# Kernel tuning notes

Hardware: AMD Instinct MI355X
Metric: run time of the kernel (lower is better)

Reference implementation:

```python
import jax, jax.numpy as jnp
import numpy as np

N = 100000          # nodes
E = 600000          # edges (avg degree ~6, mesh graph)
C_IN = 6            # input features (xyz + normals)
H = 64              # hidden channels per PointTransformerConv
OUT = 10            # out_channels
NEG_SLOPE = 0.01    # F.leaky_relu default slope
IN_DIMS = [C_IN, C_IN + H, C_IN + 2 * H, C_IN + 3 * H]


def _lin(key, fin, fout):
    return jax.random.normal(key, (fin, fout), jnp.float32) / np.float32(np.sqrt(fin))


def setup_inputs() -> dict:
    key = jax.random.key(0)
    ks = jax.random.split(key, 40)
    inp = {
        "x": jax.random.normal(ks[0], (N, C_IN), jnp.float32),
        "edge_index": jax.random.randint(ks[1], (2, E), 0, N, jnp.int32),
    }
    k = 2
    for l, fin in enumerate(IN_DIMS, start=1):
        inp[f"w{l}_lin"] = _lin(ks[k], fin, H); k += 1   # value projection (bias=False)
        inp[f"w{l}_src"] = _lin(ks[k], fin, H); k += 1   # attention src projection
        inp[f"w{l}_dst"] = _lin(ks[k], fin, H); k += 1   # attention dst projection
        inp[f"w{l}_pos"] = _lin(ks[k], fin, H); k += 1   # positional MLP (Linear)
        inp[f"b{l}_pos"] = jnp.zeros((H,), jnp.float32)
    inp["w_mlp1"] = _lin(ks[k], C_IN + 4 * H, H); k += 1
    inp["b_mlp1"] = jnp.zeros((H,), jnp.float32)
    inp["w_mlp2"] = _lin(ks[k], H, OUT); k += 1
    inp["b_mlp2"] = jnp.zeros((OUT,), jnp.float32)
    return inp


def _ptconv(x, src, dst, w_lin, w_src, w_dst, w_pos, b_pos):
    """PointTransformerConv with x serving as both features and positions.
    message = softmax_i(a_dst[i] - a_src[j] + delta_ij) * (h[j] + delta_ij),
    delta_ij = pos_nn(x_i - x_j); sum-aggregated over incoming edges."""
    h = x @ w_lin                                   # [N,H] values
    a_src = x @ w_src                               # [N,H]
    a_dst = x @ w_dst                               # [N,H]
    delta = (x[dst] - x[src]) @ w_pos + b_pos       # [E,H] pos_nn(pos_i - pos_j)
    alpha = a_dst[dst] - a_src[src] + delta         # [E,H] per-edge, per-channel logits
    # numerically stable segment softmax over edges grouped by destination node
    amax = jax.ops.segment_max(alpha, dst, num_segments=N)      # [N,H]
    e = jnp.exp(alpha - amax[dst])                              # [E,H]
    denom = jax.ops.segment_sum(e, dst, num_segments=N)         # [N,H]
    w = e / (denom[dst] + 1e-16)                                # [E,H]
    return jax.ops.segment_sum(w * (h[src] + delta), dst, num_segments=N)  # [N,H]


def _forward(x, edge_index, ps):
    src, dst = edge_index[0], edge_index[1]
    lrelu = lambda v: jnp.where(v > 0, v, NEG_SLOPE * v)
    x1 = _ptconv(x, src, dst, *ps[0])
    x2 = lrelu(_ptconv(jnp.concatenate([x, x1], 1), src, dst, *ps[1]))
    x3 = lrelu(_ptconv(jnp.concatenate([x, x1, x2], 1), src, dst, *ps[2]))
    x4 = lrelu(_ptconv(jnp.concatenate([x, x1, x2, x3], 1), src, dst, *ps[3]))
    out = jnp.concatenate([x, x1, x2, x3, x4], 1)   # [N, 262]
    w_mlp1, b_mlp1, w_mlp2, b_mlp2 = ps[4]
    out = out @ w_mlp1 + b_mlp1                     # dropout = identity (eval mode)
    return out @ w_mlp2 + b_mlp2                    # [N, OUT]


def reference(x, edge_index,
              w1_lin, w1_src, w1_dst, w1_pos, b1_pos,
              w2_lin, w2_src, w2_dst, w2_pos, b2_pos,
              w3_lin, w3_src, w3_dst, w3_pos, b3_pos,
              w4_lin, w4_src, w4_dst, w4_pos, b4_pos,
              w_mlp1, b_mlp1, w_mlp2, b_mlp2):
    ps = [(w1_lin, w1_src, w1_dst, w1_pos, b1_pos),
          (w2_lin, w2_src, w2_dst, w2_pos, b2_pos),
          (w3_lin, w3_src, w3_dst, w3_pos, b3_pos),
          (w4_lin, w4_src, w4_dst, w4_pos, b4_pos),
          (w_mlp1, b_mlp1, w_mlp2, b_mlp2)]
    return _forward(x, edge_index, ps)
```

## Files before the change

### kernel.cpp

```cpp
#include <hip/hip_runtime.h>
#include <hip/hip_fp16.h>

#define NN 100000
#define EE 600000
#define XSB 288
#define SCAN_B 2048

typedef __attribute__((ext_vector_type(8))) short s16x8;
typedef __attribute__((ext_vector_type(4))) float f32x4;

__device__ inline unsigned short f2b(float f) {
    unsigned u = __float_as_uint(f);
    u += 0x7fffu + ((u >> 16) & 1u);
    return (unsigned short)(u >> 16);
}


__global__ void k_init_x(const float* __restrict__ x, unsigned short* __restrict__ xb) {
    int idx = blockIdx.x * 256 + threadIdx.x;
    if (idx < NN * 6) {
        int i = idx / 6, c = idx - i * 6;
        xb[(size_t)i * XSB + c] = f2b(x[idx]);
    }
}

__global__ void k_wconv(const float* __restrict__ wlin, const float* __restrict__ wsrc,
                        const float* __restrict__ wpos,
                        unsigned short* __restrict__ wt, int fin, int KP) {
    int idx = blockIdx.x * 256 + threadIdx.x;
    if (idx >= 192 * KP) return;
    int ks = idx / 6144;
    int rem = idx - ks * 6144;
    int col = rem >> 5, kk = rem & 31;
    int k = ks * 32 + kk;
    float val = 0.f;
    if (k < fin) {
        int m = col >> 6, c = col & 63;
        const float* W = (m == 0) ? wlin : (m == 1) ? wsrc : wpos;
        val = W[k * 64 + c];
    }
    wt[idx] = f2b(val);
}

__global__ void k_wconv1(const float* __restrict__ w1, unsigned short* __restrict__ wt) {
    int idx = blockIdx.x * 256 + threadIdx.x;
    if (idx >= 64 * 288) return;
    int col = idx / 288, k = idx - col * 288;
    wt[idx] = f2b((k < 262) ? w1[k * 64 + col] : 0.f);
}


__global__ void k_hist(const int* __restrict__ ei, int* __restrict__ deg) {
    int e = blockIdx.x * 256 + threadIdx.x;
    if (e < EE) atomicAdd(&deg[ei[EE + e]], 1);
}

__global__ void k_scan1(const int* __restrict__ deg, int* __restrict__ rowptr,
                        int* __restrict__ bsum) {
    __shared__ int sh[256];
    int b = blockIdx.x, t = threadIdx.x;
    int base = b * SCAN_B + t * 8;
    int vals[8];
    int s = 0;
#pragma unroll
    for (int j = 0; j < 8; j++) {
        int i = base + j;
        int d = (i < NN) ? deg[i] : 0;
        s += d;
        vals[j] = s;
    }
    sh[t] = s;
    __syncthreads();
    for (int off = 1; off < 256; off <<= 1) {
        int vv = (t >= off) ? sh[t - off] : 0;
        __syncthreads();
        sh[t] += vv;
        __syncthreads();
    }
    int excl = (t > 0) ? sh[t - 1] : 0;
#pragma unroll
    for (int j = 0; j < 8; j++) {
        int i = base + j;
        if (i < NN) rowptr[i + 1] = vals[j] + excl;
    }
    if (t == 255) bsum[b] = sh[255];
}

__global__ void k_scan2(int* __restrict__ bsum, int nb) {
    __shared__ int sh[256];
    int t = threadIdx.x;
    sh[t] = (t < nb) ? bsum[t] : 0;
    __syncthreads();
    for (int off = 1; off < 256; off <<= 1) {
        int vv = (t >= off) ? sh[t - off] : 0;
        __syncthreads();
        sh[t] += vv;
        __syncthreads();
    }
    if (t < nb) bsum[t] = sh[t];
}

__global__ void k_scan3(const int* __restrict__ deg, int* __restrict__ rowptr,
                        const int* __restrict__ bsum, int* __restrict__ cursor) {
    int b = blockIdx.x, t = threadIdx.x;
    int off = (b > 0) ? bsum[b - 1] : 0;
    int base = b * SCAN_B + t * 8;
#pragma unroll
    for (int j = 0; j < 8; j++) {
        int i = base + j;
        if (i < NN) {
            int incl = rowptr[i + 1] + off;
            rowptr[i + 1] = incl;
            cursor[i] = incl - deg[i];
        }
    }
    if (b == 0 && t == 0) rowptr[0] = 0;
}

__global__ void k_scatter(const int* __restrict__ ei, int* __restrict__ cursor,
                          int* __restrict__ csrc) {
    int e = blockIdx.x * 256 + threadIdx.x;
    if (e < EE) {
        int d = ei[EE + e];
        int pos = atomicAdd(&cursor[d], 1);
        csrc[pos] = ei[e];
    }
}


template <int KP>
__global__ __launch_bounds__(256) void k_projm(
    const unsigned short* __restrict__ xb, const unsigned short* __restrict__ wt,
    const float* __restrict__ bpos,
    __half2* __restrict__ vg, float* __restrict__ q) {
    __shared__ short wl[192 * 32];
    const int t = threadIdx.x;
    const int w = t >> 6, l = t & 63;
    const int lo = l & 15, hi = l >> 4;
    const int row_w = blockIdx.x * 64 + w * 16;

    f32x4 acc[12];
#pragma unroll
    for (int i = 0; i < 12; i++) acc[i] = (f32x4)0.f;

    const unsigned short* arow = xb + (size_t)(row_w + lo) * XSB;
#pragma unroll
    for (int ks = 0; ks < KP / 32; ks++) {
        __syncthreads();
        {
            const uint4* src = (const uint4*)wt + (size_t)ks * 768;
            uint4* dst = (uint4*)wl;
#pragma unroll
            for (int i = 0; i < 3; i++) dst[i * 256 + t] = src[i * 256 + t];
        }
        __syncthreads();
        s16x8 af = *(const s16x8*)(arow + ks * 32 + hi * 8);
#pragma unroll
        for (int ct = 0; ct < 12; ct++) {
            s16x8 bf = *(const s16x8*)&wl[(ct * 16 + lo) * 32 + hi * 8];
            acc[ct] = __builtin_amdgcn_mfma_f32_16x16x32_bf16(af, bf, acc[ct], 0, 0, 0);
        }
    }

#pragma unroll
    for (int r = 0; r < 4; r++) {
        int node = row_w + hi * 4 + r;
        if (node < NN) {
#pragma unroll
            for (int j = 0; j < 4; j++) {
                int c = j * 16 + lo;
                float h  = acc[0 + j][r];
                float as = acc[4 + j][r];
                float p  = acc[8 + j][r];
                size_t o = (size_t)node * 64 + c;
                vg[o] = __floats2half2_rn(as + p, h - p);
                q[o] = p + bpos[c];
            }
        }
    }
}


__global__ __launch_bounds__(256) void k_mlp1(
    const unsigned short* __restrict__ xb, const unsigned short* __restrict__ w1t,
    const float* __restrict__ b1, float* __restrict__ hid) {
    const int w = threadIdx.x >> 6, l = threadIdx.x & 63;
    const int lo = l & 15, hi = l >> 4;
    const int row_w = blockIdx.x * 256 + w * 64;

    f32x4 acc[4][4];
#pragma unroll
    for (int a = 0; a < 4; a++)
#pragma unroll
        for (int b = 0; b < 4; b++) acc[a][b] = (f32x4)0.f;

#pragma unroll
    for (int ks = 0; ks < 9; ks++) {
        const int k0 = ks * 32 + hi * 8;
        s16x8 bf[4];
#pragma unroll
        for (int ct = 0; ct < 4; ct++)
            bf[ct] = *(const s16x8*)(w1t + (size_t)(ct * 16 + lo) * 288 + k0);
#pragma unroll
        for (int rt = 0; rt < 4; rt++) {
            s16x8 af = *(const s16x8*)(xb + (size_t)(row_w + rt * 16 + lo) * XSB + k0);
#pragma unroll
            for (int ct = 0; ct < 4; ct++)
                acc[rt][ct] = __builtin_amdgcn_mfma_f32_16x16x32_bf16(af, bf[ct], acc[rt][ct], 0, 0, 0);
        }
    }

#pragma unroll
    for (int rt = 0; rt < 4; rt++) {
#pragma unroll
        for (int r = 0; r < 4; r++) {
            int node = row_w + rt * 16 + hi * 4 + r;
            if (node < NN) {
#pragma unroll
                for (int ct = 0; ct < 4; ct++) {
                    int c = ct * 16 + lo;
                    hid[(size_t)node * 64 + c] = acc[rt][ct][r] + b1[c];
                }
            }
        }
    }
}


template <int RELU>
__global__ __launch_bounds__(256) void k_edge(
    const __half2* __restrict__ vg, const float* __restrict__ q,
    const int* __restrict__ rowptr, const int* __restrict__ csrc,
    unsigned short* __restrict__ xb, int col) {
    int node = blockIdx.x * 4 + (threadIdx.x >> 6);
    int lane = threadIdx.x & 63;
    if (node >= NN) return;
    float ql = q[(size_t)node * 64 + lane];
    int b = rowptr[node], e = rowptr[node + 1];
    float d = 0.f, s1 = 0.f;
    for (int p0 = b; p0 < e; p0 += 8) {
        int cnt = e - p0;
        int sidx[8];
#pragma unroll
        for (int j = 0; j < 8; j++) {
            int pp = p0 + j;
            if (pp >= e) pp = e - 1;
            sidx[j] = csrc[pp];
        }
        __half2 hv[8];
#pragma unroll
        for (int j = 0; j < 8; j++)
            hv[j] = vg[(size_t)sidx[j] * 64 + lane];
#pragma unroll
        for (int j = 0; j < 8; j++) {
            float2 f = __half22float2(hv[j]);
            float ee = __expf(-f.x);
            if (j >= cnt) ee = 0.f;
            d += ee;
            s1 = fmaf(ee, f.y, s1);
        }
    }
    float o = (s1 + ql * d) / (d + 1e-16f);
    if (RELU) o = (o > 0.f) ? o : 0.01f * o;
    xb[(size_t)node * XSB + col + lane] = f2b(o);
}


__global__ __launch_bounds__(256) void k_mlp2(
    const float* __restrict__ hid, const float* __restrict__ w2,
    const float* __restrict__ b2, float* __restrict__ out) {
    int n = blockIdx.x * 256 + threadIdx.x;
    if (n >= NN) return;
    float acc[10];
#pragma unroll
    for (int o = 0; o < 10; o++) acc[o] = b2[o];
    for (int h = 0; h < 64; h++) {
        float hv = hid[(size_t)n * 64 + h];
#pragma unroll
        for (int o = 0; o < 10; o++) acc[o] += hv * w2[h * 10 + o];
    }
#pragma unroll
    for (int o = 0; o < 10; o++) out[(size_t)n * 10 + o] = acc[o];
}


extern "C" void kernel_launch(void* const* d_in, const int* in_sizes, int n_in,
                              void* d_out, int out_size, void* d_ws, size_t ws_size,
                              hipStream_t stream) {
    const float* x = (const float*)d_in[0];
    const int* ei = (const int*)d_in[1];
    const float* W[4][4];
    const float* BP[4];
    int base = 2;
    for (int l = 0; l < 4; l++) {
        for (int m = 0; m < 4; m++) W[l][m] = (const float*)d_in[base + m];
        BP[l] = (const float*)d_in[base + 4];
        base += 5;
    }
    const float* w1 = (const float*)d_in[22];
    const float* b1 = (const float*)d_in[23];
    const float* w2 = (const float*)d_in[24];
    const float* b2 = (const float*)d_in[25];

    char* wsp = (char*)d_ws;
    size_t off = 0;
    auto alloc = [&](size_t bytes) {
        void* p = wsp + off;
        off += (bytes + 255) & ~(size_t)255;
        return p;
    };
    unsigned short* xb = (unsigned short*)alloc((size_t)(NN + 256) * XSB * 2);
    __half2* vg = (__half2*)alloc((size_t)NN * 64 * 4);
    float* q = (float*)alloc((size_t)NN * 64 * 4);
    int* deg = (int*)alloc((size_t)NN * 4);
    int* rowptr = (int*)alloc((size_t)(NN + 1) * 4);
    int* cursor = (int*)alloc((size_t)NN * 4);
    int* bsum = (int*)alloc(1024 * 4);
    int* csrc = (int*)alloc((size_t)EE * 4);
    const int KPv[4] = {32, 96, 160, 224};
    const int FINv[4] = {6, 70, 134, 198};
    unsigned short* wt[4];
    for (int l = 0; l < 4; l++) wt[l] = (unsigned short*)alloc((size_t)192 * KPv[l] * 2);
    unsigned short* w1t = (unsigned short*)alloc((size_t)64 * 288 * 2);
    float* hid = q;

    hipMemsetAsync(deg, 0, (size_t)NN * 4, stream);
    k_init_x<<<(NN * 6 + 255) / 256, 256, 0, stream>>>(x, xb);
    for (int l = 0; l < 4; l++)
        k_wconv<<<(192 * KPv[l] + 255) / 256, 256, 0, stream>>>(
            W[l][0], W[l][1], W[l][3], wt[l], FINv[l], KPv[l]);
    k_wconv1<<<(64 * 288 + 255) / 256, 256, 0, stream>>>(w1, w1t);

    k_hist<<<(EE + 255) / 256, 256, 0, stream>>>(ei, deg);
    int nb = (NN + SCAN_B - 1) / SCAN_B;
    k_scan1<<<nb, 256, 0, stream>>>(deg, rowptr, bsum);
    k_scan2<<<1, 256, 0, stream>>>(bsum, nb);
    k_scan3<<<nb, 256, 0, stream>>>(deg, rowptr, bsum, cursor);
    k_scatter<<<(EE + 255) / 256, 256, 0, stream>>>(ei, cursor, csrc);

    const int gProj = (NN + 63) / 64;
    const int gEdge = (NN + 3) / 4;

    k_projm<32><<<gProj, 256, 0, stream>>>(xb, wt[0], BP[0], vg, q);
    k_edge<0><<<gEdge, 256, 0, stream>>>(vg, q, rowptr, csrc, xb, 6);
    k_projm<96><<<gProj, 256, 0, stream>>>(xb, wt[1], BP[1], vg, q);
    k_edge<1><<<gEdge, 256, 0, stream>>>(vg, q, rowptr, csrc, xb, 70);
    k_projm<160><<<gProj, 256, 0, stream>>>(xb, wt[2], BP[2], vg, q);
    k_edge<1><<<gEdge, 256, 0, stream>>>(vg, q, rowptr, csrc, xb, 134);
    k_projm<224><<<gProj, 256, 0, stream>>>(xb, wt[3], BP[3], vg, q);
    k_edge<1><<<gEdge, 256, 0, stream>>>(vg, q, rowptr, csrc, xb, 198);

    k_mlp1<<<(NN + 255) / 256, 256, 0, stream>>>(xb, w1t, b1, hid);
    k_mlp2<<<(NN + 255) / 256, 256, 0, stream>>>(hid, w2, b2, (float*)d_out);
}
```

Baseline: 330.0 us.

## Fuse setup kernels, fuse MLP layers, halve q precision, widen edge loads

Merges x conversion, all weight conversions and the degree memset into one setup launch. Fuses the second MLP into the first MFMA kernel using shuffle reductions, which removes the hidden-activation round trip through memory. Stores q in fp16, processes 32 rows per wave in the projection kernel so each shared-memory weight load is reused twice, and has the edge kernel gather 8-byte vectors with half-waves covering alternate edges. The fp16 q adds some rounding error.

```diff
diff --git a/kernel.cpp b/kernel.cpp
--- a/kernel.cpp
+++ b/kernel.cpp
@@ -15,20 +15,9 @@
     return (unsigned short)(u >> 16);
 }
 
-
-__global__ void k_init_x(const float* __restrict__ x, unsigned short* __restrict__ xb) {
-    int idx = blockIdx.x * 256 + threadIdx.x;
-    if (idx < NN * 6) {
-        int i = idx / 6, c = idx - i * 6;
-        xb[(size_t)i * XSB + c] = f2b(x[idx]);
-    }
-}
-
-__global__ void k_wconv(const float* __restrict__ wlin, const float* __restrict__ wsrc,
-                        const float* __restrict__ wpos,
-                        unsigned short* __restrict__ wt, int fin, int KP) {
-    int idx = blockIdx.x * 256 + threadIdx.x;
-    if (idx >= 192 * KP) return;
+__device__ inline void wconv_elem(int idx, int fin,
+                                  const float* wlin, const float* wsrc,
+                                  const float* wpos, unsigned short* wt) {
     int ks = idx / 6144;
     int rem = idx - ks * 6144;
     int col = rem >> 5, kk = rem & 31;
@@ -42,11 +31,44 @@
     wt[idx] = f2b(val);
 }
 
-__global__ void k_wconv1(const float* __restrict__ w1, unsigned short* __restrict__ wt) {
-    int idx = blockIdx.x * 256 + threadIdx.x;
-    if (idx >= 64 * 288) return;
-    int col = idx / 288, k = idx - col * 288;
-    wt[idx] = f2b((k < 262) ? w1[k * 64 + col] : 0.f);
+#define O0 600000
+#define O1 606144
+#define O2 624576
+#define O3 655296
+#define O4 698304
+#define O5 716736
+#define O6 816736
+
+__global__ __launch_bounds__(256) void k_setup(
+    const float* __restrict__ x,
+    const float* __restrict__ wl0, const float* __restrict__ ws0, const float* __restrict__ wp0,
+    const float* __restrict__ wl1, const float* __restrict__ ws1, const float* __restrict__ wp1,
+    const float* __restrict__ wl2, const float* __restrict__ ws2, const float* __restrict__ wp2,
+    const float* __restrict__ wl3, const float* __restrict__ ws3, const float* __restrict__ wp3,
+    const float* __restrict__ w1,
+    unsigned short* __restrict__ xb,
+    unsigned short* __restrict__ wt0, unsigned short* __restrict__ wt1,
+    unsigned short* __restrict__ wt2, unsigned short* __restrict__ wt3,
+    unsigned short* __restrict__ w1t, int* __restrict__ deg) {
+    int i = blockIdx.x * 256 + threadIdx.x;
+    if (i < O0) {
+        int n = i / 6, c = i - n * 6;
+        xb[(size_t)n * XSB + c] = f2b(x[i]);
+    } else if (i < O1) {
+        wconv_elem(i - O0, 6, wl0, ws0, wp0, wt0);
+    } else if (i < O2) {
+        wconv_elem(i - O1, 70, wl1, ws1, wp1, wt1);
+    } else if (i < O3) {
+        wconv_elem(i - O2, 134, wl2, ws2, wp2, wt2);
+    } else if (i < O4) {
+        wconv_elem(i - O3, 198, wl3, ws3, wp3, wt3);
+    } else if (i < O5) {
+        int idx = i - O4;
+        int col = idx / 288, k = idx - col * 288;
+        w1t[idx] = f2b((k < 262) ? w1[k * 64 + col] : 0.f);
+    } else if (i < O6) {
+        deg[i - O5] = 0;
+    }
 }
 
 
@@ -132,18 +154,21 @@
 __global__ __launch_bounds__(256) void k_projm(
     const unsigned short* __restrict__ xb, const unsigned short* __restrict__ wt,
     const float* __restrict__ bpos,
-    __half2* __restrict__ vg, float* __restrict__ q) {
+    __half2* __restrict__ vg, __half* __restrict__ qh) {
     __shared__ short wl[192 * 32];
     const int t = threadIdx.x;
     const int w = t >> 6, l = t & 63;
     const int lo = l & 15, hi = l >> 4;
-    const int row_w = blockIdx.x * 64 + w * 16;
-
-    f32x4 acc[12];
-#pragma unroll
-    for (int i = 0; i < 12; i++) acc[i] = (f32x4)0.f;
-
-    const unsigned short* arow = xb + (size_t)(row_w + lo) * XSB;
+    const int row_w = blockIdx.x * 128 + w * 32;
+
+    f32x4 acc[2][12];
+#pragma unroll
+    for (int a = 0; a < 2; a++)
+#pragma unroll
+        for (int i = 0; i < 12; i++) acc[a][i] = (f32x4)0.f;
+
+    const unsigned short* arow0 = xb + (size_t)(row_w + lo) * XSB;
+    const unsigned short* arow1 = xb + (size_t)(row_w + 16 + lo) * XSB;
 #pragma unroll
     for (int ks = 0; ks < KP / 32; ks++) {
         __syncthreads();
@@ -154,36 +179,52 @@
             for (int i = 0; i < 3; i++) dst[i * 256 + t] = src[i * 256 + t];
         }
         __syncthreads();
-        s16x8 af = *(const s16x8*)(arow + ks * 32 + hi * 8);
+        s16x8 af0 = *(const s16x8*)(arow0 + ks * 32 + hi * 8);
+        s16x8 af1 = *(const s16x8*)(arow1 + ks * 32 + hi * 8);
 #pragma unroll
         for (int ct = 0; ct < 12; ct++) {
             s16x8 bf = *(const s16x8*)&wl[(ct * 16 + lo) * 32 + hi * 8];
-            acc[ct] = __builtin_amdgcn_mfma_f32_16x16x32_bf16(af, bf, acc[ct], 0, 0, 0);
-        }
-    }
-
-#pragma unroll
-    for (int r = 0; r < 4; r++) {
-        int node = row_w + hi * 4 + r;
-        if (node < NN) {
-#pragma unroll
-            for (int j = 0; j < 4; j++) {
-                int c = j * 16 + lo;
-                float h  = acc[0 + j][r];
-                float as = acc[4 + j][r];
-                float p  = acc[8 + j][r];
-                size_t o = (size_t)node * 64 + c;
-                vg[o] = __floats2half2_rn(as + p, h - p);
-                q[o] = p + bpos[c];
+            acc[0][ct] = __builtin_amdgcn_mfma_f32_16x16x32_bf16(af0, bf, acc[0][ct], 0, 0, 0);
+            acc[1][ct] = __builtin_amdgcn_mfma_f32_16x16x32_bf16(af1, bf, acc[1][ct], 0, 0, 0);
+        }
+    }
+
+#pragma unroll
+    for (int tile = 0; tile < 2; tile++) {
+#pragma unroll
+        for (int r = 0; r < 4; r++) {
+            int node = row_w + tile * 16 + hi * 4 + r;
+            if (node < NN) {
+#pragma unroll
+                for (int j = 0; j < 4; j++) {
+                    int c = j * 16 + lo;
+                    float h  = acc[tile][0 + j][r];
+                    float as = acc[tile][4 + j][r];
+                    float p  = acc[tile][8 + j][r];
+                    size_t o = (size_t)node * 64 + c;
+                    vg[o] = __floats2half2_rn(as + p, h - p);
+                    qh[o] = __float2half(p + bpos[c]);
+                }
             }
         }
     }
 }
 
 
-__global__ __launch_bounds__(256) void k_mlp1(
+__global__ __launch_bounds__(256) void k_mlp1f(
     const unsigned short* __restrict__ xb, const unsigned short* __restrict__ w1t,
-    const float* __restrict__ b1, float* __restrict__ hid) {
+    const float* __restrict__ b1, const float* __restrict__ w2,
+    const float* __restrict__ b2, float* __restrict__ out) {
+    __shared__ float w2l[64][10];
+    __shared__ float b2l[10];
+    __shared__ float b1l[64];
+    for (int t = threadIdx.x; t < 714; t += 256) {
+        if (t < 640) ((float*)w2l)[t] = w2[t];
+        else if (t < 650) b2l[t - 640] = b2[t - 640];
+        else b1l[t - 650] = b1[t - 650];
+    }
+    __syncthreads();
+
     const int w = threadIdx.x >> 6, l = threadIdx.x & 63;
     const int lo = l & 15, hi = l >> 4;
     const int row_w = blockIdx.x * 256 + w * 64;
@@ -215,12 +256,26 @@
 #pragma unroll
         for (int r = 0; r < 4; r++) {
             int node = row_w + rt * 16 + hi * 4 + r;
-            if (node < NN) {
-#pragma unroll
-                for (int ct = 0; ct < 4; ct++) {
-                    int c = ct * 16 + lo;
-                    hid[(size_t)node * 64 + c] = acc[rt][ct][r] + b1[c];
-                }
+            float po[10];
+#pragma unroll
+            for (int o = 0; o < 10; o++) po[o] = 0.f;
+#pragma unroll
+            for (int ct = 0; ct < 4; ct++) {
+                int c = ct * 16 + lo;
+                float hv = acc[rt][ct][r] + b1l[c];
+#pragma unroll
+                for (int o = 0; o < 10; o++) po[o] = fmaf(hv, w2l[c][o], po[o]);
+            }
+#pragma unroll
+            for (int m = 1; m < 16; m <<= 1)
+#pragma unroll
+                for (int o = 0; o < 10; o++) po[o] += __shfl_xor(po[o], m);
+            if (lo == 0 && node < NN) {
+                float* op = out + (size_t)node * 10;
+#pragma unroll
+                for (int o = 0; o < 5; o++)
+                    *(float2*)(op + o * 2) = make_float2(po[o * 2] + b2l[o * 2],
+                                                         po[o * 2 + 1] + b2l[o * 2 + 1]);
             }
         }
     }
@@ -229,58 +284,53 @@
 
 template <int RELU>
 __global__ __launch_bounds__(256) void k_edge(
-    const __half2* __restrict__ vg, const float* __restrict__ q,
+    const uint2* __restrict__ vg,
+    const __half2* __restrict__ qh,
     const int* __restrict__ rowptr, const int* __restrict__ csrc,
     unsigned short* __restrict__ xb, int col) {
     int node = blockIdx.x * 4 + (threadIdx.x >> 6);
-    int lane = threadIdx.x & 63;
+    int l = threadIdx.x & 63;
+    int h = l >> 5, lp = l & 31;
     if (node >= NN) return;
-    float ql = q[(size_t)node * 64 + lane];
     int b = rowptr[node], e = rowptr[node + 1];
-    float d = 0.f, s1 = 0.f;
+    float d0 = 0.f, d1 = 0.f, s0 = 0.f, s1 = 0.f;
     for (int p0 = b; p0 < e; p0 += 8) {
         int cnt = e - p0;
-        int sidx[8];
-#pragma unroll
-        for (int j = 0; j < 8; j++) {
-            int pp = p0 + j;
+        int sidx[4];
+#pragma unroll
+        for (int t = 0; t < 4; t++) {
+            int pp = p0 + 2 * t + h;
             if (pp >= e) pp = e - 1;
-            sidx[j] = csrc[pp];
-        }
-        __half2 hv[8];
-#pragma unroll
-        for (int j = 0; j < 8; j++)
-            hv[j] = vg[(size_t)sidx[j] * 64 + lane];
-#pragma unroll
-        for (int j = 0; j < 8; j++) {
-            float2 f = __half22float2(hv[j]);
-            float ee = __expf(-f.x);
-            if (j >= cnt) ee = 0.f;
-            d += ee;
-            s1 = fmaf(ee, f.y, s1);
-        }
-    }
-    float o = (s1 + ql * d) / (d + 1e-16f);
-    if (RELU) o = (o > 0.f) ? o : 0.01f * o;
-    xb[(size_t)node * XSB + col + lane] = f2b(o);
-}
-
-
-__global__ __launch_bounds__(256) void k_mlp2(
-    const float* __restrict__ hid, const float* __restrict__ w2,
-    const float* __restrict__ b2, float* __restrict__ out) {
-    int n = blockIdx.x * 256 + threadIdx.x;
-    if (n >= NN) return;
-    float acc[10];
-#pragma unroll
-    for (int o = 0; o < 10; o++) acc[o] = b2[o];
-    for (int h = 0; h < 64; h++) {
-        float hv = hid[(size_t)n * 64 + h];
-#pragma unroll
-        for (int o = 0; o < 10; o++) acc[o] += hv * w2[h * 10 + o];
-    }
-#pragma unroll
-    for (int o = 0; o < 10; o++) out[(size_t)n * 10 + o] = acc[o];
+            sidx[t] = csrc[pp];
+        }
+        uint2 gv[4];
+#pragma unroll
+        for (int t = 0; t < 4; t++)
+            gv[t] = vg[(size_t)sidx[t] * 32 + lp];
+#pragma unroll
+        for (int t = 0; t < 4; t++) {
+            bool ok = (2 * t + h) < cnt;
+            float2 f0 = __half22float2(*(const __half2*)&gv[t].x);
+            float2 f1 = __half22float2(*(const __half2*)&gv[t].y);
+            float e0 = ok ? __expf(-f0.x) : 0.f;
+            float e1 = ok ? __expf(-f1.x) : 0.f;
+            d0 += e0; s0 = fmaf(e0, f0.y, s0);
+            d1 += e1; s1 = fmaf(e1, f1.y, s1);
+        }
+    }
+    d0 += __shfl_xor(d0, 32); d1 += __shfl_xor(d1, 32);
+    s0 += __shfl_xor(s0, 32); s1 += __shfl_xor(s1, 32);
+    if (h == 0) {
+        float2 qf = __half22float2(qh[(size_t)node * 32 + lp]);
+        float o0 = (s0 + qf.x * d0) / (d0 + 1e-16f);
+        float o1 = (s1 + qf.y * d1) / (d1 + 1e-16f);
+        if (RELU) {
+            o0 = (o0 > 0.f) ? o0 : 0.01f * o0;
+            o1 = (o1 > 0.f) ? o1 : 0.01f * o1;
+        }
+        unsigned pack = (unsigned)f2b(o0) | ((unsigned)f2b(o1) << 16);
+        *(unsigned*)&xb[(size_t)node * XSB + col + 2 * lp] = pack;
+    }
 }
 
 
@@ -311,25 +361,21 @@
     };
     unsigned short* xb = (unsigned short*)alloc((size_t)(NN + 256) * XSB * 2);
     __half2* vg = (__half2*)alloc((size_t)NN * 64 * 4);
-    float* q = (float*)alloc((size_t)NN * 64 * 4);
+    __half* qh = (__half*)alloc((size_t)NN * 64 * 2);
     int* deg = (int*)alloc((size_t)NN * 4);
     int* rowptr = (int*)alloc((size_t)(NN + 1) * 4);
     int* cursor = (int*)alloc((size_t)NN * 4);
     int* bsum = (int*)alloc(1024 * 4);
     int* csrc = (int*)alloc((size_t)EE * 4);
     const int KPv[4] = {32, 96, 160, 224};
-    const int FINv[4] = {6, 70, 134, 198};
     unsigned short* wt[4];
     for (int l = 0; l < 4; l++) wt[l] = (unsigned short*)alloc((size_t)192 * KPv[l] * 2);
     unsigned short* w1t = (unsigned short*)alloc((size_t)64 * 288 * 2);
-    float* hid = q;
-
-    hipMemsetAsync(deg, 0, (size_t)NN * 4, stream);
-    k_init_x<<<(NN * 6 + 255) / 256, 256, 0, stream>>>(x, xb);
-    for (int l = 0; l < 4; l++)
-        k_wconv<<<(192 * KPv[l] + 255) / 256, 256, 0, stream>>>(
-            W[l][0], W[l][1], W[l][3], wt[l], FINv[l], KPv[l]);
-    k_wconv1<<<(64 * 288 + 255) / 256, 256, 0, stream>>>(w1, w1t);
+
+    k_setup<<<(O6 + 255) / 256, 256, 0, stream>>>(
+        x, W[0][0], W[0][1], W[0][3], W[1][0], W[1][1], W[1][3],
+        W[2][0], W[2][1], W[2][3], W[3][0], W[3][1], W[3][3], w1,
+        xb, wt[0], wt[1], wt[2], wt[3], w1t, deg);
 
     k_hist<<<(EE + 255) / 256, 256, 0, stream>>>(ei, deg);
     int nb = (NN + SCAN_B - 1) / SCAN_B;
@@ -338,18 +384,19 @@
     k_scan3<<<nb, 256, 0, stream>>>(deg, rowptr, bsum, cursor);
     k_scatter<<<(EE + 255) / 256, 256, 0, stream>>>(ei, cursor, csrc);
 
-    const int gProj = (NN + 63) / 64;
+    const int gProj = (NN + 127) / 128;
     const int gEdge = (NN + 3) / 4;
-
-    k_projm<32><<<gProj, 256, 0, stream>>>(xb, wt[0], BP[0], vg, q);
-    k_edge<0><<<gEdge, 256, 0, stream>>>(vg, q, rowptr, csrc, xb, 6);
-    k_projm<96><<<gProj, 256, 0, stream>>>(xb, wt[1], BP[1], vg, q);
-    k_edge<1><<<gEdge, 256, 0, stream>>>(vg, q, rowptr, csrc, xb, 70);
-    k_projm<160><<<gProj, 256, 0, stream>>>(xb, wt[2], BP[2], vg, q);
-    k_edge<1><<<gEdge, 256, 0, stream>>>(vg, q, rowptr, csrc, xb, 134);
-    k_projm<224><<<gProj, 256, 0, stream>>>(xb, wt[3], BP[3], vg, q);
-    k_edge<1><<<gEdge, 256, 0, stream>>>(vg, q, rowptr, csrc, xb, 198);
-
-    k_mlp1<<<(NN + 255) / 256, 256, 0, stream>>>(xb, w1t, b1, hid);
-    k_mlp2<<<(NN + 255) / 256, 256, 0, stream>>>(hid, w2, b2, (float*)d_out);
-}
+    const uint2* vgu = (const uint2*)vg;
+    const __half2* qh2 = (const __half2*)qh;
+
+    k_projm<32><<<gProj, 256, 0, stream>>>(xb, wt[0], BP[0], vg, qh);
+    k_edge<0><<<gEdge, 256, 0, stream>>>(vgu, qh2, rowptr, csrc, xb, 6);
+    k_projm<96><<<gProj, 256, 0, stream>>>(xb, wt[1], BP[1], vg, qh);
+    k_edge<1><<<gEdge, 256, 0, stream>>>(vgu, qh2, rowptr, csrc, xb, 70);
+    k_projm<160><<<gProj, 256, 0, stream>>>(xb, wt[2], BP[2], vg, qh);
+    k_edge<1><<<gEdge, 256, 0, stream>>>(vgu, qh2, rowptr, csrc, xb, 134);
+    k_projm<224><<<gProj, 256, 0, stream>>>(xb, wt[3], BP[3], vg, qh);
+    k_edge<1><<<gEdge, 256, 0, stream>>>(vgu, qh2, rowptr, csrc, xb, 198);
+
+    k_mlp1f<<<(NN + 255) / 256, 256, 0, stream>>>(xb, w1t, b1, w2, b2, (float*)d_out);
+}
```

Result: slower. 338.9 us (+2.7%).
